# Optimization experiments

Hardware: AMD Instinct MI355X
Metric: run time of the kernel (lower is better)

The kernel has to match this reference:

```python
import jax, jax.numpy as jnp
import numpy as np

N_NODES = 50000
N_EDGES = 640000
D_IN = 128
D_HID = 128
D_OUT = 128
N_GRAPHS = 64


def gcn_conv(x, edge_index, W, b, n_nodes):
    """PyG GCNConv: D^{-1/2} (A + I) D^{-1/2} X W + b (unit edge weights)."""
    src, dst = edge_index[0], edge_index[1]
    h = x @ W  # [N, d_out]
    # degree counts target-side edges plus the self loop
    deg = jax.ops.segment_sum(jnp.ones_like(dst, dtype=h.dtype), dst,
                              num_segments=n_nodes) + 1.0
    dinv = jax.lax.rsqrt(deg)  # deg >= 1 so always finite
    norm = dinv[src] * dinv[dst]  # [E]
    msg = h[src] * norm[:, None]  # gather + scale  [E, d_out]
    agg = jax.ops.segment_sum(msg, dst, num_segments=n_nodes)
    # self-loop contribution: norm_ii = dinv_i^2
    agg = agg + h * (dinv * dinv)[:, None]
    return agg + b


def global_mean_pool(x, batch, n_graphs):
    sums = jax.ops.segment_sum(x, batch, num_segments=n_graphs)
    cnt = jax.ops.segment_sum(jnp.ones((x.shape[0],), dtype=x.dtype), batch,
                              num_segments=n_graphs)
    return sums / jnp.maximum(cnt, 1.0)[:, None]


def setup_inputs() -> dict:
    key = jax.random.key(0)
    k = jax.random.split(key, 8)
    x = jax.random.normal(k[0], (N_NODES, D_IN), dtype=jnp.float32)
    edge_index = jax.random.randint(k[1], (2, N_EDGES), 0, N_NODES, dtype=jnp.int64)
    batch = jnp.sort(jax.random.randint(k[2], (N_NODES,), 0, N_GRAPHS, dtype=jnp.int64))
    s1 = 1.0 / np.sqrt(D_IN)
    s2 = 1.0 / np.sqrt(D_HID)
    W1 = jax.random.uniform(k[3], (D_IN, D_HID), jnp.float32, -s1, s1)
    b1 = jnp.zeros((D_HID,), jnp.float32)
    W2 = jax.random.uniform(k[4], (D_HID, D_OUT), jnp.float32, -s2, s2)
    b2 = jnp.zeros((D_OUT,), jnp.float32)
    return {"x": x, "edge_index": edge_index, "batch": batch,
            "W1": W1, "b1": b1, "W2": W2, "b2": b2}


def reference(x, edge_index, batch, W1, b1, W2, b2):
    n = x.shape[0]
    h = jax.nn.relu(gcn_conv(x, edge_index, W1, b1, n))
    h = gcn_conv(h, edge_index, W2, b2, n)
    return global_mean_pool(h, batch, N_GRAPHS)
```

## Files before the change

kernel.cpp:

```cpp
#include <hip/hip_runtime.h>


#define D 128
#define NGRAPH 64
#define SCAN_B 1024
#define AGG_BLOCKS 2048

typedef _Float16 h16x2 __attribute__((ext_vector_type(2)));
typedef _Float16 f16x8 __attribute__((ext_vector_type(8)));
typedef float    f32x4 __attribute__((ext_vector_type(4)));

__device__ __forceinline__ float2 h2f(unsigned u) {
    h16x2 h = __builtin_bit_cast(h16x2, u);
    return make_float2((float)h.x, (float)h.y);
}
__device__ __forceinline__ unsigned f2h(float x, float y) {
    h16x2 h;
    h.x = (_Float16)x;
    h.y = (_Float16)y;
    return __builtin_bit_cast(unsigned, h);
}

__global__ void zero_out_kernel(float* __restrict__ out, int n) {
    int i = blockIdx.x * blockDim.x + threadIdx.x;
    if (i < n) out[i] = 0.f;
}

__global__ __launch_bounds__(256) void conv_count_kernel(const float* __restrict__ X,
                                                         _Float16* __restrict__ Xh,
                                                         const float* __restrict__ W1,
                                                         _Float16* __restrict__ WB,
                                                         const int* __restrict__ ei,
                                                         int* __restrict__ deg,
                                                         int N, int E, int cb) {
    int b = (int)blockIdx.x;
    if (b < cb) {
        int idx = b * 256 + (int)threadIdx.x;
        int total = N * (D / 4);
        if (idx < total) {
            float4 v = ((const float4*)X)[idx];
            uint2 o;
            o.x = f2h(v.x, v.y);
            o.y = f2h(v.z, v.w);
            ((uint2*)Xh)[idx] = o;
        }
        return;
    }
    if (b < cb + 8) {
        int idx = (b - cb) * 256 + (int)threadIdx.x;
        int lane = idx & 63;
        int nt   = (idx >> 6) & 7;
        int kt   = idx >> 9;
        int col  = nt * 16 + (lane & 15);
        int krow = kt * 32 + (lane >> 4) * 8;
#pragma unroll
        for (int j = 0; j < 8; ++j)
            WB[idx * 8 + j] = (_Float16)W1[(krow + j) * D + col];
        return;
    }
    int e = (b - cb - 8) * 256 + (int)threadIdx.x;
    if (e < E) {
        int d = ei[E + e];
        if (d >= 0 && d < N) atomicAdd(&deg[d], 1);
    }
}

__global__ __launch_bounds__(SCAN_B) void block_scan_kernel(const int* __restrict__ deg,
                                                            int* __restrict__ rowstart,
                                                            int* __restrict__ bsum,
                                                            float* __restrict__ dinv,
                                                            int N) {
    __shared__ int sc[SCAN_B];
    int t = threadIdx.x;
    int i = blockIdx.x * SCAN_B + t;
    int orig = (i < N) ? deg[i] : 0;
    int v = orig;
    sc[t] = v;
    __syncthreads();
    for (int off = 1; off < SCAN_B; off <<= 1) {
        int add = (t >= off) ? sc[t - off] : 0;
        __syncthreads();
        v += add;
        sc[t] = v;
        __syncthreads();
    }
    if (i < N) {
        rowstart[i] = v - orig;
        dinv[i]     = rsqrtf((float)orig + 1.0f);
    }
    if (t == SCAN_B - 1) bsum[blockIdx.x] = v;
}

__global__ __launch_bounds__(SCAN_B) void finalize_scan_kernel(const int* __restrict__ bsum,
                                                               int* __restrict__ rowstart,
                                                               int* __restrict__ cursor,
                                                               int N, int nblk, int E) {
    __shared__ int s_off;
    if (threadIdx.x < 64) {
        int lane = (int)threadIdx.x;
        int v = (lane < nblk && lane < (int)blockIdx.x) ? bsum[lane] : 0;
        for (int off = 32; off > 0; off >>= 1) v += __shfl_down(v, off);
        if (lane == 0) s_off = v;
    }
    __syncthreads();
    int i = blockIdx.x * SCAN_B + threadIdx.x;
    if (i < N) {
        int rs = rowstart[i] + s_off;
        rowstart[i] = rs;
        cursor[i]   = rs;
    }
    if (blockIdx.x == 0 && threadIdx.x == 0) rowstart[N] = E;
}

__global__ void fill_kernel(const int* __restrict__ ei, int* __restrict__ cursor,
                            int* __restrict__ colidx, int E, int N) {
    int e = blockIdx.x * blockDim.x + threadIdx.x;
    if (e < E) {
        int d = ei[E + e];
        if (d >= 0 && d < N) {
            int slot = atomicAdd(&cursor[d], 1);
            if (slot >= 0 && slot < E) {
                int s = ei[e];
                colidx[slot] = min(max(s, 0), N - 1);
            }
        }
    }
}

__global__ __launch_bounds__(256) void gemm_kernel(const _Float16* __restrict__ Xh,
                                                   const _Float16* __restrict__ WB,
                                                   const float* __restrict__ dinv,
                                                   _Float16* __restrict__ Gh,
                                                   int N) {
    int t = (int)threadIdx.x;
    int wave = t >> 6, lane = t & 63;
    int mbase = blockIdx.x * 64 + wave * 16;
    int arow  = mbase + (lane & 15);
    if (arow >= N) arow = N - 1;
    int kgrp  = lane >> 4;

    f16x8 afrag[4];
#pragma unroll
    for (int kt = 0; kt < 4; ++kt) {
        uint4 u = *(const uint4*)(Xh + (size_t)arow * D + kt * 32 + kgrp * 8);
        afrag[kt] = __builtin_bit_cast(f16x8, u);
    }
    f32x4 acc[8];
#pragma unroll
    for (int nt = 0; nt < 8; ++nt) acc[nt] = (f32x4){0.f, 0.f, 0.f, 0.f};
#pragma unroll
    for (int kt = 0; kt < 4; ++kt) {
#pragma unroll
        for (int nt = 0; nt < 8; ++nt) {
            uint4 u = *(const uint4*)(WB + (((kt * 8 + nt) * 64 + lane) * 8));
            f16x8 bfrag = __builtin_bit_cast(f16x8, u);
            acc[nt] = __builtin_amdgcn_mfma_f32_16x16x32_f16(afrag[kt], bfrag, acc[nt], 0, 0, 0);
        }
    }
    int r0 = mbase + kgrp * 4;
#pragma unroll
    for (int r = 0; r < 4; ++r) {
        int row = r0 + r;
        if (row < N) {
            float dv = dinv[row];
#pragma unroll
            for (int nt = 0; nt < 8; ++nt)
                Gh[(size_t)row * D + nt * 16 + (lane & 15)] = (_Float16)(dv * acc[nt][r]);
        }
    }
}

__global__ __launch_bounds__(256) void agg1_kernel(const unsigned* __restrict__ Gh,
                                                   const int* __restrict__ rowstart,
                                                   const int* __restrict__ colidx,
                                                   const float* __restrict__ dinv,
                                                   const float* __restrict__ b1,
                                                   unsigned* __restrict__ Hh,
                                                   int N, int chunk) {
    int gid  = blockIdx.x * 4 + (threadIdx.x >> 6);
    int lane = threadIdx.x & 63;
    int i0 = gid * chunk, i1 = min(i0 + chunk, N);
    float bx = b1[2 * lane], by = b1[2 * lane + 1];
    for (int i = i0; i < i1; ++i) {
        float di = dinv[i];
        float2 acc = h2f(Gh[(size_t)i * (D / 2) + lane]);
        int e0 = rowstart[i], e1 = rowstart[i + 1];
        int e = e0;
        for (; e + 7 < e1; e += 8) {
            unsigned u[8];
#pragma unroll
            for (int j = 0; j < 8; ++j)
                u[j] = Gh[(size_t)colidx[e + j] * (D / 2) + lane];
#pragma unroll
            for (int j = 0; j < 8; ++j) {
                float2 v = h2f(u[j]);
                acc.x += v.x;
                acc.y += v.y;
            }
        }
        for (; e + 3 < e1; e += 4) {
            unsigned u[4];
#pragma unroll
            for (int j = 0; j < 4; ++j)
                u[j] = Gh[(size_t)colidx[e + j] * (D / 2) + lane];
#pragma unroll
            for (int j = 0; j < 4; ++j) {
                float2 v = h2f(u[j]);
                acc.x += v.x;
                acc.y += v.y;
            }
        }
        for (; e < e1; ++e) {
            float2 v = h2f(Gh[(size_t)colidx[e] * (D / 2) + lane]);
            acc.x += v.x;
            acc.y += v.y;
        }
        float hx = fmaxf(fmaf(di, acc.x, bx), 0.f) * di;
        float hy = fmaxf(fmaf(di, acc.y, by), 0.f) * di;
        Hh[(size_t)i * (D / 2) + lane] = f2h(hx, hy);
    }
}

__global__ __launch_bounds__(256) void agg2_pool_kernel(const unsigned* __restrict__ Hh,
                                                        const int* __restrict__ rowstart,
                                                        const int* __restrict__ colidx,
                                                        const float* __restrict__ dinv,
                                                        const int* __restrict__ batch,
                                                        float* __restrict__ pool,
                                                        int N, int chunk) {
    int gid  = blockIdx.x * 4 + (threadIdx.x >> 6);
    int lane = threadIdx.x & 63;
    int i0 = gid * chunk, i1 = min(i0 + chunk, N);
    if (i0 >= N) return;

    float2 pa = make_float2(0.f, 0.f);
    int cur = min(max(batch[i0], 0), NGRAPH - 1);
    for (int i = i0; i < i1; ++i) {
        float di = dinv[i];
        float2 a = h2f(Hh[(size_t)i * (D / 2) + lane]);
        int e0 = rowstart[i], e1 = rowstart[i + 1];
        int e = e0;
        for (; e + 7 < e1; e += 8) {
            unsigned u[8];
#pragma unroll
            for (int j = 0; j < 8; ++j)
                u[j] = Hh[(size_t)colidx[e + j] * (D / 2) + lane];
#pragma unroll
            for (int j = 0; j < 8; ++j) {
                float2 v = h2f(u[j]);
                a.x += v.x;
                a.y += v.y;
            }
        }
        for (; e + 3 < e1; e += 4) {
            unsigned u[4];
#pragma unroll
            for (int j = 0; j < 4; ++j)
                u[j] = Hh[(size_t)colidx[e + j] * (D / 2) + lane];
#pragma unroll
            for (int j = 0; j < 4; ++j) {
                float2 v = h2f(u[j]);
                a.x += v.x;
                a.y += v.y;
            }
        }
        for (; e < e1; ++e) {
            float2 v = h2f(Hh[(size_t)colidx[e] * (D / 2) + lane]);
            a.x += v.x;
            a.y += v.y;
        }
        int b = min(max(batch[i], 0), NGRAPH - 1);
        if (b != cur) {
            atomicAdd(&pool[(size_t)cur * D + 2 * lane], pa.x);
            atomicAdd(&pool[(size_t)cur * D + 2 * lane + 1], pa.y);
            pa = make_float2(0.f, 0.f);
            cur = b;
        }
        pa.x = fmaf(di, a.x, pa.x);
        pa.y = fmaf(di, a.y, pa.y);
    }
    atomicAdd(&pool[(size_t)cur * D + 2 * lane], pa.x);
    atomicAdd(&pool[(size_t)cur * D + 2 * lane + 1], pa.y);
}

__device__ __forceinline__ int lbound(const int* __restrict__ a, int n, int v) {
    int lo = 0, hi = n;
    while (lo < hi) {
        int m = (lo + hi) >> 1;
        if (a[m] < v) lo = m + 1; else hi = m;
    }
    return lo;
}

__global__ void final_gemm_kernel(const float* __restrict__ pool,
                                  const int* __restrict__ batch,
                                  const float* __restrict__ W2,
                                  const float* __restrict__ b2,
                                  float* __restrict__ out, int N) {
    int g = blockIdx.x, o = threadIdx.x;
    int s = lbound(batch, N, g);
    int e = lbound(batch, N, g + 1);
    float inv_cnt = 1.0f / fmaxf((float)(e - s), 1.0f);
    float acc = 0.f;
#pragma unroll 4
    for (int k = 0; k < D; ++k)
        acc = fmaf(pool[g * D + k], W2[k * D + o], acc);
    out[g * D + o] = acc * inv_cnt + b2[o];
}


extern "C" void kernel_launch(void* const* d_in, const int* in_sizes, int n_in,
                              void* d_out, int out_size, void* d_ws, size_t ws_size,
                              hipStream_t stream) {
    const float* x     = (const float*)d_in[0];
    const int*   ei    = (const int*)  d_in[1];
    const int*   batch = (const int*)  d_in[2];
    const float* W1    = (const float*)d_in[3];
    const float* b1    = (const float*)d_in[4];
    const float* W2    = (const float*)d_in[5];
    const float* b2    = (const float*)d_in[6];
    float* out = (float*)d_out;

    const int N = in_sizes[0] / D;
    const int E = in_sizes[1] / 2;
    const int nblk = (N + SCAN_B - 1) / SCAN_B;

    char* ws = (char*)d_ws;
    size_t off = 0;
    auto carve = [&](size_t bytes) {
        size_t o = off;
        off = (off + bytes + 255) & ~(size_t)255;
        return o;
    };
    size_t o_deg      = carve((size_t)N * 4);
    size_t o_pool     = carve((size_t)NGRAPH * D * 4);
    size_t zspan      = off;
    size_t o_rowstart = carve((size_t)(N + 1) * 4);
    size_t o_cursor   = carve((size_t)(N + 1) * 4);
    size_t o_dinv     = carve((size_t)N * 4);
    size_t o_colidx   = carve((size_t)E * 4);
    size_t o_bsum     = carve((size_t)64 * 4);
    size_t o_xh       = carve((size_t)N * D * 2);
    size_t o_wb       = carve((size_t)D * D * 2);
    size_t o_gh       = carve((size_t)N * D * 2);
    size_t o_hh       = carve((size_t)N * D * 2);
    size_t need = off;

    if (ws_size < need) {
        zero_out_kernel<<<(out_size + 255) / 256, 256, 0, stream>>>(out, out_size);
        return;
    }

    int*       deg      = (int*)      (ws + o_deg);
    float*     pool     = (float*)    (ws + o_pool);
    int*       rowstart = (int*)      (ws + o_rowstart);
    int*       cursor   = (int*)      (ws + o_cursor);
    float*     dinv     = (float*)    (ws + o_dinv);
    int*       colidx   = (int*)      (ws + o_colidx);
    int*       bsum     = (int*)      (ws + o_bsum);
    _Float16*  Xh       = (_Float16*) (ws + o_xh);
    _Float16*  WB       = (_Float16*) (ws + o_wb);
    _Float16*  Gh       = (_Float16*) (ws + o_gh);
    _Float16*  Hh       = (_Float16*) (ws + o_hh);

    hipMemsetAsync(ws, 0, zspan, stream);

    int eb = (E + 255) / 256;
    int gb = (N + 63) / 64;
    int cb = (N * (D / 4) + 255) / 256;

    conv_count_kernel<<<cb + 8 + eb, 256, 0, stream>>>(x, Xh, W1, WB, ei, deg, N, E, cb);
    block_scan_kernel<<<nblk, SCAN_B, 0, stream>>>(deg, rowstart, bsum, dinv, N);
    finalize_scan_kernel<<<nblk, SCAN_B, 0, stream>>>(bsum, rowstart, cursor, N, nblk, E);
    fill_kernel<<<eb, 256, 0, stream>>>(ei, cursor, colidx, E, N);
    gemm_kernel<<<gb, 256, 0, stream>>>(Xh, WB, dinv, Gh, N);

    int groups = AGG_BLOCKS * 4;
    int chunk  = (N + groups - 1) / groups;
    agg1_kernel<<<AGG_BLOCKS, 256, 0, stream>>>((const unsigned*)Gh, rowstart, colidx,
                                                dinv, b1, (unsigned*)Hh, N, chunk);
    agg2_pool_kernel<<<AGG_BLOCKS, 256, 0, stream>>>((const unsigned*)Hh, rowstart, colidx,
                                                     dinv, batch, pool, N, chunk);
    final_gemm_kernel<<<NGRAPH, D, 0, stream>>>(pool, batch, W2, b2, out, N);
}
```

Before: 233.0 us.

## Split feature matrices into two 64-column planes and drop fill-stage atomics

Gh and Hh are stored as two column-halves of 64 fp16 values each, so every gathered neighbor row in the aggregation kernels is 128 bytes. The aggregation loops now run twice, once per half, with one fp16 per lane instead of a packed pair. The intent is to shrink the per-pass working set so each half fits better in cache during the random gathers. The CSR fill stage also records each edge's atomic rank in the degree-count pass and computes its slot as rowstart plus rank, which removes the cursor array and the second round of atomics, at the cost of an extra E-sized rank buffer. Nontemporal stores are added for Gh and Hh.

```diff
diff --git a/kernel.cpp b/kernel.cpp
--- a/kernel.cpp
+++ b/kernel.cpp
@@ -10,10 +10,6 @@
 typedef _Float16 f16x8 __attribute__((ext_vector_type(8)));
 typedef float    f32x4 __attribute__((ext_vector_type(4)));
 
-__device__ __forceinline__ float2 h2f(unsigned u) {
-    h16x2 h = __builtin_bit_cast(h16x2, u);
-    return make_float2((float)h.x, (float)h.y);
-}
 __device__ __forceinline__ unsigned f2h(float x, float y) {
     h16x2 h;
     h.x = (_Float16)x;
@@ -32,6 +28,7 @@
                                                          _Float16* __restrict__ WB,
                                                          const int* __restrict__ ei,
                                                          int* __restrict__ deg,
+                                                         int* __restrict__ rank,
                                                          int N, int E, int cb) {
     int b = (int)blockIdx.x;
     if (b < cb) {
@@ -61,7 +58,7 @@
     int e = (b - cb - 8) * 256 + (int)threadIdx.x;
     if (e < E) {
         int d = ei[E + e];
-        if (d >= 0 && d < N) atomicAdd(&deg[d], 1);
+        if (d >= 0 && d < N) rank[e] = atomicAdd(&deg[d], 1);
     }
 }
 
@@ -93,7 +90,6 @@
 
 __global__ __launch_bounds__(SCAN_B) void finalize_scan_kernel(const int* __restrict__ bsum,
                                                                int* __restrict__ rowstart,
-                                                               int* __restrict__ cursor,
                                                                int N, int nblk, int E) {
     __shared__ int s_off;
     if (threadIdx.x < 64) {
@@ -104,21 +100,19 @@
     }
     __syncthreads();
     int i = blockIdx.x * SCAN_B + threadIdx.x;
-    if (i < N) {
-        int rs = rowstart[i] + s_off;
-        rowstart[i] = rs;
-        cursor[i]   = rs;
-    }
+    if (i < N) rowstart[i] += s_off;
     if (blockIdx.x == 0 && threadIdx.x == 0) rowstart[N] = E;
 }
 
-__global__ void fill_kernel(const int* __restrict__ ei, int* __restrict__ cursor,
+__global__ void fill_kernel(const int* __restrict__ ei,
+                            const int* __restrict__ rowstart,
+                            const int* __restrict__ rank,
                             int* __restrict__ colidx, int E, int N) {
     int e = blockIdx.x * blockDim.x + threadIdx.x;
     if (e < E) {
         int d = ei[E + e];
         if (d >= 0 && d < N) {
-            int slot = atomicAdd(&cursor[d], 1);
+            int slot = rowstart[d] + rank[e];
             if (slot >= 0 && slot < E) {
                 int s = ei[e];
                 colidx[slot] = min(max(s, 0), N - 1);
@@ -164,64 +158,62 @@
         if (row < N) {
             float dv = dinv[row];
 #pragma unroll
-            for (int nt = 0; nt < 8; ++nt)
-                Gh[(size_t)row * D + nt * 16 + (lane & 15)] = (_Float16)(dv * acc[nt][r]);
-        }
-    }
-}
-
-__global__ __launch_bounds__(256) void agg1_kernel(const unsigned* __restrict__ Gh,
+            for (int nt = 0; nt < 8; ++nt) {
+                int p   = nt >> 2;
+                int pos = (nt & 3) * 16 + (lane & 15);
+                _Float16 v = (_Float16)(dv * acc[nt][r]);
+                __builtin_nontemporal_store(v, Gh + ((size_t)p * N + row) * 64 + pos);
+            }
+        }
+    }
+}
+
+__global__ __launch_bounds__(256) void agg1_kernel(const _Float16* __restrict__ Gh,
                                                    const int* __restrict__ rowstart,
                                                    const int* __restrict__ colidx,
                                                    const float* __restrict__ dinv,
                                                    const float* __restrict__ b1,
-                                                   unsigned* __restrict__ Hh,
+                                                   _Float16* __restrict__ Hh,
                                                    int N, int chunk) {
     int gid  = blockIdx.x * 4 + (threadIdx.x >> 6);
     int lane = threadIdx.x & 63;
     int i0 = gid * chunk, i1 = min(i0 + chunk, N);
-    float bx = b1[2 * lane], by = b1[2 * lane + 1];
-    for (int i = i0; i < i1; ++i) {
-        float di = dinv[i];
-        float2 acc = h2f(Gh[(size_t)i * (D / 2) + lane]);
-        int e0 = rowstart[i], e1 = rowstart[i + 1];
-        int e = e0;
-        for (; e + 7 < e1; e += 8) {
-            unsigned u[8];
-#pragma unroll
-            for (int j = 0; j < 8; ++j)
-                u[j] = Gh[(size_t)colidx[e + j] * (D / 2) + lane];
-#pragma unroll
-            for (int j = 0; j < 8; ++j) {
-                float2 v = h2f(u[j]);
-                acc.x += v.x;
-                acc.y += v.y;
-            }
-        }
-        for (; e + 3 < e1; e += 4) {
-            unsigned u[4];
-#pragma unroll
-            for (int j = 0; j < 4; ++j)
-                u[j] = Gh[(size_t)colidx[e + j] * (D / 2) + lane];
-#pragma unroll
-            for (int j = 0; j < 4; ++j) {
-                float2 v = h2f(u[j]);
-                acc.x += v.x;
-                acc.y += v.y;
-            }
-        }
-        for (; e < e1; ++e) {
-            float2 v = h2f(Gh[(size_t)colidx[e] * (D / 2) + lane]);
-            acc.x += v.x;
-            acc.y += v.y;
-        }
-        float hx = fmaxf(fmaf(di, acc.x, bx), 0.f) * di;
-        float hy = fmaxf(fmaf(di, acc.y, by), 0.f) * di;
-        Hh[(size_t)i * (D / 2) + lane] = f2h(hx, hy);
-    }
-}
-
-__global__ __launch_bounds__(256) void agg2_pool_kernel(const unsigned* __restrict__ Hh,
+    if (i0 >= N) return;
+#pragma unroll
+    for (int p = 0; p < 2; ++p) {
+        const _Float16* G = Gh + (size_t)p * N * 64;
+        _Float16*       H = Hh + (size_t)p * N * 64;
+        float bv = b1[p * 64 + lane];
+        for (int i = i0; i < i1; ++i) {
+            float di = dinv[i];
+            float acc = (float)G[(size_t)i * 64 + lane];
+            int e0 = rowstart[i], e1 = rowstart[i + 1];
+            int e = e0;
+            for (; e + 7 < e1; e += 8) {
+                _Float16 u[8];
+#pragma unroll
+                for (int j = 0; j < 8; ++j)
+                    u[j] = G[(size_t)colidx[e + j] * 64 + lane];
+#pragma unroll
+                for (int j = 0; j < 8; ++j) acc += (float)u[j];
+            }
+            for (; e + 3 < e1; e += 4) {
+                _Float16 u[4];
+#pragma unroll
+                for (int j = 0; j < 4; ++j)
+                    u[j] = G[(size_t)colidx[e + j] * 64 + lane];
+#pragma unroll
+                for (int j = 0; j < 4; ++j) acc += (float)u[j];
+            }
+            for (; e < e1; ++e)
+                acc += (float)G[(size_t)colidx[e] * 64 + lane];
+            float h = fmaxf(fmaf(di, acc, bv), 0.f) * di;
+            __builtin_nontemporal_store((_Float16)h, H + (size_t)i * 64 + lane);
+        }
+    }
+}
+
+__global__ __launch_bounds__(256) void agg2_pool_kernel(const _Float16* __restrict__ Hh,
                                                         const int* __restrict__ rowstart,
                                                         const int* __restrict__ colidx,
                                                         const float* __restrict__ dinv,
@@ -232,55 +224,44 @@
     int lane = threadIdx.x & 63;
     int i0 = gid * chunk, i1 = min(i0 + chunk, N);
     if (i0 >= N) return;
-
-    float2 pa = make_float2(0.f, 0.f);
-    int cur = min(max(batch[i0], 0), NGRAPH - 1);
-    for (int i = i0; i < i1; ++i) {
-        float di = dinv[i];
-        float2 a = h2f(Hh[(size_t)i * (D / 2) + lane]);
-        int e0 = rowstart[i], e1 = rowstart[i + 1];
-        int e = e0;
-        for (; e + 7 < e1; e += 8) {
-            unsigned u[8];
-#pragma unroll
-            for (int j = 0; j < 8; ++j)
-                u[j] = Hh[(size_t)colidx[e + j] * (D / 2) + lane];
-#pragma unroll
-            for (int j = 0; j < 8; ++j) {
-                float2 v = h2f(u[j]);
-                a.x += v.x;
-                a.y += v.y;
-            }
-        }
-        for (; e + 3 < e1; e += 4) {
-            unsigned u[4];
-#pragma unroll
-            for (int j = 0; j < 4; ++j)
-                u[j] = Hh[(size_t)colidx[e + j] * (D / 2) + lane];
-#pragma unroll
-            for (int j = 0; j < 4; ++j) {
-                float2 v = h2f(u[j]);
-                a.x += v.x;
-                a.y += v.y;
-            }
-        }
-        for (; e < e1; ++e) {
-            float2 v = h2f(Hh[(size_t)colidx[e] * (D / 2) + lane]);
-            a.x += v.x;
-            a.y += v.y;
-        }
-        int b = min(max(batch[i], 0), NGRAPH - 1);
-        if (b != cur) {
-            atomicAdd(&pool[(size_t)cur * D + 2 * lane], pa.x);
-            atomicAdd(&pool[(size_t)cur * D + 2 * lane + 1], pa.y);
-            pa = make_float2(0.f, 0.f);
-            cur = b;
-        }
-        pa.x = fmaf(di, a.x, pa.x);
-        pa.y = fmaf(di, a.y, pa.y);
-    }
-    atomicAdd(&pool[(size_t)cur * D + 2 * lane], pa.x);
-    atomicAdd(&pool[(size_t)cur * D + 2 * lane + 1], pa.y);
+#pragma unroll
+    for (int p = 0; p < 2; ++p) {
+        const _Float16* H = Hh + (size_t)p * N * 64;
+        float pa = 0.f;
+        int cur = min(max(batch[i0], 0), NGRAPH - 1);
+        for (int i = i0; i < i1; ++i) {
+            float di = dinv[i];
+            float a = (float)H[(size_t)i * 64 + lane];
+            int e0 = rowstart[i], e1 = rowstart[i + 1];
+            int e = e0;
+            for (; e + 7 < e1; e += 8) {
+                _Float16 u[8];
+#pragma unroll
+                for (int j = 0; j < 8; ++j)
+                    u[j] = H[(size_t)colidx[e + j] * 64 + lane];
+#pragma unroll
+                for (int j = 0; j < 8; ++j) a += (float)u[j];
+            }
+            for (; e + 3 < e1; e += 4) {
+                _Float16 u[4];
+#pragma unroll
+                for (int j = 0; j < 4; ++j)
+                    u[j] = H[(size_t)colidx[e + j] * 64 + lane];
+#pragma unroll
+                for (int j = 0; j < 4; ++j) a += (float)u[j];
+            }
+            for (; e < e1; ++e)
+                a += (float)H[(size_t)colidx[e] * 64 + lane];
+            int b = min(max(batch[i], 0), NGRAPH - 1);
+            if (b != cur) {
+                atomicAdd(&pool[(size_t)cur * D + p * 64 + lane], pa);
+                pa = 0.f;
+                cur = b;
+            }
+            pa = fmaf(di, a, pa);
+        }
+        atomicAdd(&pool[(size_t)cur * D + p * 64 + lane], pa);
+    }
 }
 
 __device__ __forceinline__ int lbound(const int* __restrict__ a, int n, int v) {
@@ -336,9 +317,9 @@
     size_t o_pool     = carve((size_t)NGRAPH * D * 4);
     size_t zspan      = off;
     size_t o_rowstart = carve((size_t)(N + 1) * 4);
-    size_t o_cursor   = carve((size_t)(N + 1) * 4);
     size_t o_dinv     = carve((size_t)N * 4);
     size_t o_colidx   = carve((size_t)E * 4);
+    size_t o_rank     = carve((size_t)E * 4);
     size_t o_bsum     = carve((size_t)64 * 4);
     size_t o_xh       = carve((size_t)N * D * 2);
     size_t o_wb       = carve((size_t)D * D * 2);
@@ -354,9 +335,9 @@
     int*       deg      = (int*)      (ws + o_deg);
     float*     pool     = (float*)    (ws + o_pool);
     int*       rowstart = (int*)      (ws + o_rowstart);
-    int*       cursor   = (int*)      (ws + o_cursor);
     float*     dinv     = (float*)    (ws + o_dinv);
     int*       colidx   = (int*)      (ws + o_colidx);
+    int*       rank     = (int*)      (ws + o_rank);
     int*       bsum     = (int*)      (ws + o_bsum);
     _Float16*  Xh       = (_Float16*) (ws + o_xh);
     _Float16*  WB       = (_Float16*) (ws + o_wb);
@@ -369,17 +350,18 @@
     int gb = (N + 63) / 64;
     int cb = (N * (D / 4) + 255) / 256;
 
-    conv_count_kernel<<<cb + 8 + eb, 256, 0, stream>>>(x, Xh, W1, WB, ei, deg, N, E, cb);
+    conv_count_kernel<<<cb + 8 + eb, 256, 0, stream>>>(x, Xh, W1, WB, ei, deg, rank,
+                                                       N, E, cb);
     block_scan_kernel<<<nblk, SCAN_B, 0, stream>>>(deg, rowstart, bsum, dinv, N);
-    finalize_scan_kernel<<<nblk, SCAN_B, 0, stream>>>(bsum, rowstart, cursor, N, nblk, E);
-    fill_kernel<<<eb, 256, 0, stream>>>(ei, cursor, colidx, E, N);
+    finalize_scan_kernel<<<nblk, SCAN_B, 0, stream>>>(bsum, rowstart, N, nblk, E);
+    fill_kernel<<<eb, 256, 0, stream>>>(ei, rowstart, rank, colidx, E, N);
     gemm_kernel<<<gb, 256, 0, stream>>>(Xh, WB, dinv, Gh, N);
 
     int groups = AGG_BLOCKS * 4;
     int chunk  = (N + groups - 1) / groups;
-    agg1_kernel<<<AGG_BLOCKS, 256, 0, stream>>>((const unsigned*)Gh, rowstart, colidx,
-                                                dinv, b1, (unsigned*)Hh, N, chunk);
-    agg2_pool_kernel<<<AGG_BLOCKS, 256, 0, stream>>>((const unsigned*)Hh, rowstart, colidx,
-                                                     dinv, batch, pool, N, chunk);
+    agg1_kernel<<<AGG_BLOCKS, 256, 0, stream>>>(Gh, rowstart, colidx, dinv, b1,
+                                                Hh, N, chunk);
+    agg2_pool_kernel<<<AGG_BLOCKS, 256, 0, stream>>>(Hh, rowstart, colidx, dinv,
+                                                     batch, pool, N, chunk);
     final_gemm_kernel<<<NGRAPH, D, 0, stream>>>(pool, batch, W2, b2, out, N);
 }
```

New measurement: 251.5 us. +7.9%, slower.

## Bucket CSR edges by source range and interleave gathers across nodes by bucket

Applied to the files above, without the earlier changes.

Edge counting now records a per-edge rank within a (destination, source-bucket) counter, so the CSR fill becomes deterministic without a second atomic pass, and each row's neighbours are grouped into 8 source-range buckets. The aggregation kernels process a fixed chunk of 5 nodes per wave and walk bucket by bucket across all of them, so concurrent gathers hit a narrower source range and should get better L2 locality. Intermediate feature stores use nontemporal hints. The cost is an extra rank array, 8x larger degree and rowstart arrays, more register state per wave, and more launched blocks.

```diff
diff --git a/kernel.cpp b/kernel.cpp
--- a/kernel.cpp
+++ b/kernel.cpp
@@ -4,7 +4,9 @@
 #define D 128
 #define NGRAPH 64
 #define SCAN_B 1024
-#define AGG_BLOCKS 2048
+#define NB 8
+#define BSHIFT 13
+#define CHUNK 5
 
 typedef _Float16 h16x2 __attribute__((ext_vector_type(2)));
 typedef _Float16 f16x8 __attribute__((ext_vector_type(8)));
@@ -31,7 +33,8 @@
                                                          const float* __restrict__ W1,
                                                          _Float16* __restrict__ WB,
                                                          const int* __restrict__ ei,
-                                                         int* __restrict__ deg,
+                                                         int* __restrict__ degB,
+                                                         int* __restrict__ rank,
                                                          int N, int E, int cb) {
     int b = (int)blockIdx.x;
     if (b < cb) {
@@ -61,11 +64,15 @@
     int e = (b - cb - 8) * 256 + (int)threadIdx.x;
     if (e < E) {
         int d = ei[E + e];
-        if (d >= 0 && d < N) atomicAdd(&deg[d], 1);
-    }
-}
-
-__global__ __launch_bounds__(SCAN_B) void block_scan_kernel(const int* __restrict__ deg,
+        int s = ei[e];
+        if (d >= 0 && d < N) {
+            s = min(max(s, 0), N - 1);
+            rank[e] = atomicAdd(&degB[d * NB + (s >> BSHIFT)], 1);
+        }
+    }
+}
+
+__global__ __launch_bounds__(SCAN_B) void block_scan_kernel(const int* __restrict__ degB,
                                                             int* __restrict__ rowstart,
                                                             int* __restrict__ bsum,
                                                             float* __restrict__ dinv,
@@ -73,7 +80,11 @@
     __shared__ int sc[SCAN_B];
     int t = threadIdx.x;
     int i = blockIdx.x * SCAN_B + t;
-    int orig = (i < N) ? deg[i] : 0;
+    int orig = 0;
+    if (i < N) {
+#pragma unroll
+        for (int b = 0; b < NB; ++b) orig += degB[i * NB + b];
+    }
     int v = orig;
     sc[t] = v;
     __syncthreads();
@@ -92,8 +103,9 @@
 }
 
 __global__ __launch_bounds__(SCAN_B) void finalize_scan_kernel(const int* __restrict__ bsum,
-                                                               int* __restrict__ rowstart,
-                                                               int* __restrict__ cursor,
+                                                               const int* __restrict__ degB,
+                                                               const int* __restrict__ rowstart,
+                                                               int* __restrict__ rowstart4,
                                                                int N, int nblk, int E) {
     __shared__ int s_off;
     if (threadIdx.x < 64) {
@@ -105,24 +117,28 @@
     __syncthreads();
     int i = blockIdx.x * SCAN_B + threadIdx.x;
     if (i < N) {
-        int rs = rowstart[i] + s_off;
-        rowstart[i] = rs;
-        cursor[i]   = rs;
-    }
-    if (blockIdx.x == 0 && threadIdx.x == 0) rowstart[N] = E;
-}
-
-__global__ void fill_kernel(const int* __restrict__ ei, int* __restrict__ cursor,
+        int base = rowstart[i] + s_off;
+        int pre = 0;
+#pragma unroll
+        for (int b = 0; b < NB; ++b) {
+            rowstart4[i * NB + b] = base + pre;
+            pre += degB[i * NB + b];
+        }
+    }
+    if (blockIdx.x == 0 && threadIdx.x == 0) rowstart4[(size_t)N * NB] = E;
+}
+
+__global__ void fill_kernel(const int* __restrict__ ei,
+                            const int* __restrict__ rowstart4,
+                            const int* __restrict__ rank,
                             int* __restrict__ colidx, int E, int N) {
     int e = blockIdx.x * blockDim.x + threadIdx.x;
     if (e < E) {
         int d = ei[E + e];
         if (d >= 0 && d < N) {
-            int slot = atomicAdd(&cursor[d], 1);
-            if (slot >= 0 && slot < E) {
-                int s = ei[e];
-                colidx[slot] = min(max(s, 0), N - 1);
-            }
+            int s = min(max(ei[e], 0), N - 1);
+            int slot = rowstart4[d * NB + (s >> BSHIFT)] + rank[e];
+            if (slot >= 0 && slot < E) colidx[slot] = s;
         }
     }
 }
@@ -164,120 +180,136 @@
         if (row < N) {
             float dv = dinv[row];
 #pragma unroll
-            for (int nt = 0; nt < 8; ++nt)
-                Gh[(size_t)row * D + nt * 16 + (lane & 15)] = (_Float16)(dv * acc[nt][r]);
+            for (int nt = 0; nt < 8; ++nt) {
+                _Float16 v = (_Float16)(dv * acc[nt][r]);
+                __builtin_nontemporal_store(v, Gh + (size_t)row * D + nt * 16 + (lane & 15));
+            }
         }
     }
 }
 
 __global__ __launch_bounds__(256) void agg1_kernel(const unsigned* __restrict__ Gh,
-                                                   const int* __restrict__ rowstart,
+                                                   const int* __restrict__ rs4,
                                                    const int* __restrict__ colidx,
                                                    const float* __restrict__ dinv,
                                                    const float* __restrict__ b1,
                                                    unsigned* __restrict__ Hh,
-                                                   int N, int chunk) {
+                                                   int N) {
     int gid  = blockIdx.x * 4 + (threadIdx.x >> 6);
     int lane = threadIdx.x & 63;
-    int i0 = gid * chunk, i1 = min(i0 + chunk, N);
+    int i0 = gid * CHUNK;
+    if (i0 >= N) return;
+    int cnt = min(CHUNK, N - i0);
+
+    int bnd[CHUNK][NB];
+    int bndEnd[CHUNK];
+    float2 acc[CHUNK];
+#pragma unroll
+    for (int c = 0; c < CHUNK; ++c) {
+        int i = (c < cnt) ? (i0 + c) : i0;
+#pragma unroll
+        for (int b = 0; b < NB; ++b) bnd[c][b] = rs4[i * NB + b];
+        bndEnd[c] = rs4[i * NB + NB];
+        acc[c] = h2f(Gh[(size_t)i * 64 + lane]);
+    }
+#pragma unroll
+    for (int b = 0; b < NB; ++b) {
+#pragma unroll
+        for (int c = 0; c < CHUNK; ++c) {
+            int e  = bnd[c][b];
+            int e1 = (b < NB - 1) ? bnd[c][b + 1] : bndEnd[c];
+            for (; e + 3 < e1; e += 4) {
+                unsigned u0 = Gh[(size_t)colidx[e] * 64 + lane];
+                unsigned u1 = Gh[(size_t)colidx[e + 1] * 64 + lane];
+                unsigned u2 = Gh[(size_t)colidx[e + 2] * 64 + lane];
+                unsigned u3 = Gh[(size_t)colidx[e + 3] * 64 + lane];
+                float2 v0 = h2f(u0), v1 = h2f(u1), v2 = h2f(u2), v3 = h2f(u3);
+                acc[c].x += (v0.x + v1.x) + (v2.x + v3.x);
+                acc[c].y += (v0.y + v1.y) + (v2.y + v3.y);
+            }
+            for (; e < e1; ++e) {
+                float2 v = h2f(Gh[(size_t)colidx[e] * 64 + lane]);
+                acc[c].x += v.x;
+                acc[c].y += v.y;
+            }
+        }
+    }
     float bx = b1[2 * lane], by = b1[2 * lane + 1];
-    for (int i = i0; i < i1; ++i) {
-        float di = dinv[i];
-        float2 acc = h2f(Gh[(size_t)i * (D / 2) + lane]);
-        int e0 = rowstart[i], e1 = rowstart[i + 1];
-        int e = e0;
-        for (; e + 7 < e1; e += 8) {
-            unsigned u[8];
-#pragma unroll
-            for (int j = 0; j < 8; ++j)
-                u[j] = Gh[(size_t)colidx[e + j] * (D / 2) + lane];
-#pragma unroll
-            for (int j = 0; j < 8; ++j) {
-                float2 v = h2f(u[j]);
-                acc.x += v.x;
-                acc.y += v.y;
-            }
-        }
-        for (; e + 3 < e1; e += 4) {
-            unsigned u[4];
-#pragma unroll
-            for (int j = 0; j < 4; ++j)
-                u[j] = Gh[(size_t)colidx[e + j] * (D / 2) + lane];
-#pragma unroll
-            for (int j = 0; j < 4; ++j) {
-                float2 v = h2f(u[j]);
-                acc.x += v.x;
-                acc.y += v.y;
-            }
-        }
-        for (; e < e1; ++e) {
-            float2 v = h2f(Gh[(size_t)colidx[e] * (D / 2) + lane]);
-            acc.x += v.x;
-            acc.y += v.y;
-        }
-        float hx = fmaxf(fmaf(di, acc.x, bx), 0.f) * di;
-        float hy = fmaxf(fmaf(di, acc.y, by), 0.f) * di;
-        Hh[(size_t)i * (D / 2) + lane] = f2h(hx, hy);
+#pragma unroll
+    for (int c = 0; c < CHUNK; ++c) {
+        if (c < cnt) {
+            int i = i0 + c;
+            float di = dinv[i];
+            float hx = fmaxf(fmaf(di, acc[c].x, bx), 0.f) * di;
+            float hy = fmaxf(fmaf(di, acc[c].y, by), 0.f) * di;
+            __builtin_nontemporal_store(f2h(hx, hy), Hh + (size_t)i * 64 + lane);
+        }
     }
 }
 
 __global__ __launch_bounds__(256) void agg2_pool_kernel(const unsigned* __restrict__ Hh,
-                                                        const int* __restrict__ rowstart,
+                                                        const int* __restrict__ rs4,
                                                         const int* __restrict__ colidx,
                                                         const float* __restrict__ dinv,
                                                         const int* __restrict__ batch,
                                                         float* __restrict__ pool,
-                                                        int N, int chunk) {
+                                                        int N) {
     int gid  = blockIdx.x * 4 + (threadIdx.x >> 6);
     int lane = threadIdx.x & 63;
-    int i0 = gid * chunk, i1 = min(i0 + chunk, N);
+    int i0 = gid * CHUNK;
     if (i0 >= N) return;
-
+    int cnt = min(CHUNK, N - i0);
+
+    int bnd[CHUNK][NB];
+    int bndEnd[CHUNK];
+    float2 acc[CHUNK];
+#pragma unroll
+    for (int c = 0; c < CHUNK; ++c) {
+        int i = (c < cnt) ? (i0 + c) : i0;
+#pragma unroll
+        for (int b = 0; b < NB; ++b) bnd[c][b] = rs4[i * NB + b];
+        bndEnd[c] = rs4[i * NB + NB];
+        acc[c] = h2f(Hh[(size_t)i * 64 + lane]);
+    }
+#pragma unroll
+    for (int b = 0; b < NB; ++b) {
+#pragma unroll
+        for (int c = 0; c < CHUNK; ++c) {
+            int e  = bnd[c][b];
+            int e1 = (b < NB - 1) ? bnd[c][b + 1] : bndEnd[c];
+            for (; e + 3 < e1; e += 4) {
+                unsigned u0 = Hh[(size_t)colidx[e] * 64 + lane];
+                unsigned u1 = Hh[(size_t)colidx[e + 1] * 64 + lane];
+                unsigned u2 = Hh[(size_t)colidx[e + 2] * 64 + lane];
+                unsigned u3 = Hh[(size_t)colidx[e + 3] * 64 + lane];
+                float2 v0 = h2f(u0), v1 = h2f(u1), v2 = h2f(u2), v3 = h2f(u3);
+                acc[c].x += (v0.x + v1.x) + (v2.x + v3.x);
+                acc[c].y += (v0.y + v1.y) + (v2.y + v3.y);
+            }
+            for (; e < e1; ++e) {
+                float2 v = h2f(Hh[(size_t)colidx[e] * 64 + lane]);
+                acc[c].x += v.x;
+                acc[c].y += v.y;
+            }
+        }
+    }
     float2 pa = make_float2(0.f, 0.f);
     int cur = min(max(batch[i0], 0), NGRAPH - 1);
-    for (int i = i0; i < i1; ++i) {
-        float di = dinv[i];
-        float2 a = h2f(Hh[(size_t)i * (D / 2) + lane]);
-        int e0 = rowstart[i], e1 = rowstart[i + 1];
-        int e = e0;
-        for (; e + 7 < e1; e += 8) {
-            unsigned u[8];
-#pragma unroll
-            for (int j = 0; j < 8; ++j)
-                u[j] = Hh[(size_t)colidx[e + j] * (D / 2) + lane];
-#pragma unroll
-            for (int j = 0; j < 8; ++j) {
-                float2 v = h2f(u[j]);
-                a.x += v.x;
-                a.y += v.y;
-            }
-        }
-        for (; e + 3 < e1; e += 4) {
-            unsigned u[4];
-#pragma unroll
-            for (int j = 0; j < 4; ++j)
-                u[j] = Hh[(size_t)colidx[e + j] * (D / 2) + lane];
-#pragma unroll
-            for (int j = 0; j < 4; ++j) {
-                float2 v = h2f(u[j]);
-                a.x += v.x;
-                a.y += v.y;
-            }
-        }
-        for (; e < e1; ++e) {
-            float2 v = h2f(Hh[(size_t)colidx[e] * (D / 2) + lane]);
-            a.x += v.x;
-            a.y += v.y;
-        }
-        int b = min(max(batch[i], 0), NGRAPH - 1);
-        if (b != cur) {
-            atomicAdd(&pool[(size_t)cur * D + 2 * lane], pa.x);
-            atomicAdd(&pool[(size_t)cur * D + 2 * lane + 1], pa.y);
-            pa = make_float2(0.f, 0.f);
-            cur = b;
-        }
-        pa.x = fmaf(di, a.x, pa.x);
-        pa.y = fmaf(di, a.y, pa.y);
+#pragma unroll
+    for (int c = 0; c < CHUNK; ++c) {
+        if (c < cnt) {
+            int i = i0 + c;
+            float di = dinv[i];
+            int b = min(max(batch[i], 0), NGRAPH - 1);
+            if (b != cur) {
+                atomicAdd(&pool[(size_t)cur * D + 2 * lane], pa.x);
+                atomicAdd(&pool[(size_t)cur * D + 2 * lane + 1], pa.y);
+                pa = make_float2(0.f, 0.f);
+                cur = b;
+            }
+            pa.x = fmaf(di, acc[c].x, pa.x);
+            pa.y = fmaf(di, acc[c].y, pa.y);
+        }
     }
     atomicAdd(&pool[(size_t)cur * D + 2 * lane], pa.x);
     atomicAdd(&pool[(size_t)cur * D + 2 * lane + 1], pa.y);
@@ -332,13 +364,14 @@
         off = (off + bytes + 255) & ~(size_t)255;
         return o;
     };
-    size_t o_deg      = carve((size_t)N * 4);
+    size_t o_degB     = carve((size_t)N * NB * 4);
     size_t o_pool     = carve((size_t)NGRAPH * D * 4);
     size_t zspan      = off;
     size_t o_rowstart = carve((size_t)(N + 1) * 4);
-    size_t o_cursor   = carve((size_t)(N + 1) * 4);
+    size_t o_rs4      = carve(((size_t)N * NB + 1) * 4);
     size_t o_dinv     = carve((size_t)N * 4);
     size_t o_colidx   = carve((size_t)E * 4);
+    size_t o_rank     = carve((size_t)E * 4);
     size_t o_bsum     = carve((size_t)64 * 4);
     size_t o_xh       = carve((size_t)N * D * 2);
     size_t o_wb       = carve((size_t)D * D * 2);
@@ -351,12 +384,13 @@
         return;
     }
 
-    int*       deg      = (int*)      (ws + o_deg);
+    int*       degB     = (int*)      (ws + o_degB);
     float*     pool     = (float*)    (ws + o_pool);
     int*       rowstart = (int*)      (ws + o_rowstart);
-    int*       cursor   = (int*)      (ws + o_cursor);
+    int*       rs4      = (int*)      (ws + o_rs4);
     float*     dinv     = (float*)    (ws + o_dinv);
     int*       colidx   = (int*)      (ws + o_colidx);
+    int*       rank     = (int*)      (ws + o_rank);
     int*       bsum     = (int*)      (ws + o_bsum);
     _Float16*  Xh       = (_Float16*) (ws + o_xh);
     _Float16*  WB       = (_Float16*) (ws + o_wb);
@@ -369,17 +403,18 @@
     int gb = (N + 63) / 64;
     int cb = (N * (D / 4) + 255) / 256;
 
-    conv_count_kernel<<<cb + 8 + eb, 256, 0, stream>>>(x, Xh, W1, WB, ei, deg, N, E, cb);
-    block_scan_kernel<<<nblk, SCAN_B, 0, stream>>>(deg, rowstart, bsum, dinv, N);
-    finalize_scan_kernel<<<nblk, SCAN_B, 0, stream>>>(bsum, rowstart, cursor, N, nblk, E);
-    fill_kernel<<<eb, 256, 0, stream>>>(ei, cursor, colidx, E, N);
+    conv_count_kernel<<<cb + 8 + eb, 256, 0, stream>>>(x, Xh, W1, WB, ei, degB, rank,
+                                                       N, E, cb);
+    block_scan_kernel<<<nblk, SCAN_B, 0, stream>>>(degB, rowstart, bsum, dinv, N);
+    finalize_scan_kernel<<<nblk, SCAN_B, 0, stream>>>(bsum, degB, rowstart, rs4,
+                                                      N, nblk, E);
+    fill_kernel<<<eb, 256, 0, stream>>>(ei, rs4, rank, colidx, E, N);
     gemm_kernel<<<gb, 256, 0, stream>>>(Xh, WB, dinv, Gh, N);
 
-    int groups = AGG_BLOCKS * 4;
-    int chunk  = (N + groups - 1) / groups;
-    agg1_kernel<<<AGG_BLOCKS, 256, 0, stream>>>((const unsigned*)Gh, rowstart, colidx,
-                                                dinv, b1, (unsigned*)Hh, N, chunk);
-    agg2_pool_kernel<<<AGG_BLOCKS, 256, 0, stream>>>((const unsigned*)Hh, rowstart, colidx,
-                                                     dinv, batch, pool, N, chunk);
+    int ab = (N + 4 * CHUNK - 1) / (4 * CHUNK);
+    agg1_kernel<<<ab, 256, 0, stream>>>((const unsigned*)Gh, rs4, colidx, dinv, b1,
+                                        (unsigned*)Hh, N);
+    agg2_pool_kernel<<<ab, 256, 0, stream>>>((const unsigned*)Hh, rs4, colidx, dinv,
+                                             batch, pool, N);
     final_gemm_kernel<<<NGRAPH, D, 0, stream>>>(pool, batch, W2, b2, out, N);
 }
```

Result: slower. 305.0 us (+30.9%).
